# Optimization experiments

Measured on AMD Instinct MI355X. Metric: run time of the kernel, lower is better.

Reference implementation:

```python
import jax, jax.numpy as jnp
import numpy as np

NUM_HEADS = 8
SPLIT = 2  # split_size; idx=0 -> H_sp=H, W_sp=SPLIT (horizontal stripes)


def setup_inputs() -> dict:
    key = jax.random.key(0)
    k1, k2, k3 = jax.random.split(key, 3)
    B, C, H, W = 4, 64, 128, 128
    temp = jax.random.normal(k1, (B, 3, C, H, W), dtype=jnp.float32)
    conv_w = jax.random.normal(k2, (C, 1, 3, 3), dtype=jnp.float32) * 0.1  # depthwise OIHW
    conv_b = jax.random.normal(k3, (C,), dtype=jnp.float32) * 0.1
    return {"temp": temp, "conv_w": conv_w, "conv_b": conv_b}


def reference(temp, conv_w, conv_b):
    B, _, C, H, W = temp.shape
    hd = C // NUM_HEADS
    scale = hd ** (-0.5)
    H_sp, W_sp = H, SPLIT  # idx == 0

    # symmetric pad to multiples of window size (faithful to original; zero here)
    H_pad = (H_sp - H % H_sp) % H_sp
    W_pad = (W_sp - W % W_sp) % W_sp
    top, left = H_pad // 2, W_pad // 2
    x = jnp.pad(temp, ((0, 0), (0, 0), (0, 0), (top, H_pad - top), (left, W_pad - left)))
    H_, W_ = H + H_pad, W + W_pad
    q, k, v = x[:, 0], x[:, 1], x[:, 2]  # each [B,C,H_,W_]

    nW = (H_ // H_sp) * (W_ // W_sp)
    N = H_sp * W_sp  # tokens per window

    def im2cswin(t):
        # [B,C,H_,W_] -> [B*nW, heads, N, hd]
        w = t.reshape(B, C, H_ // H_sp, H_sp, W_ // W_sp, W_sp)
        w = w.transpose(0, 2, 4, 3, 5, 1).reshape(-1, N, C)
        return w.reshape(-1, N, NUM_HEADS, hd).transpose(0, 2, 1, 3)

    qh = im2cswin(q) * scale
    kh = im2cswin(k)

    # v windows as images [B*nW, C, H_sp, W_sp] for depthwise LePE conv
    vw = v.reshape(B, C, H_ // H_sp, H_sp, W_ // W_sp, W_sp)
    vw = vw.transpose(0, 2, 4, 1, 3, 5).reshape(-1, C, H_sp, W_sp)
    rpe = jax.lax.conv_general_dilated(
        vw, conv_w, window_strides=(1, 1), padding='SAME',
        feature_group_count=C, dimension_numbers=('NCHW', 'OIHW', 'NCHW'))
    rpe = rpe + conv_b[None, :, None, None]

    vh = vw.reshape(-1, NUM_HEADS, hd, N).transpose(0, 1, 3, 2)    # [B*nW,h,N,hd]
    rpeh = rpe.reshape(-1, NUM_HEADS, hd, N).transpose(0, 1, 3, 2)

    attn = jax.nn.softmax(jnp.einsum('whnd,whmd->whnm', qh, kh), axis=-1)
    out = jnp.einsum('whnm,whmd->whnd', attn, vh) + rpeh           # [B*nW,h,N,hd]

    out = out.transpose(0, 2, 1, 3).reshape(-1, N, C)              # [B*nW,N,C]
    # windows2img + crop
    out = out.reshape(B, H_ // H_sp, W_ // W_sp, H_sp, W_sp, C)
    out = out.transpose(0, 1, 3, 2, 4, 5).reshape(B, H_, W_, C)
    out = out[:, top:H + top, left:W + left, :]
    return out.reshape(B, H * W, C)
```

## Files before the change

### kernel.cpp

```cpp
#include <hip/hip_runtime.h>
#include <hip/hip_bf16.h>
#include <stdint.h>


typedef __attribute__((ext_vector_type(8))) short bf16x8;
typedef __attribute__((ext_vector_type(4))) short bf16x4;
typedef __attribute__((ext_vector_type(4))) float f32x4;

static __device__ __forceinline__ uint32_t pk2(float x, float y) {
    union { __hip_bfloat162 h2; uint32_t u; } c;
    c.h2 = __float22bfloat162_rn(make_float2(x, y));
    return c.u;
}
static __device__ __forceinline__ float bflo(uint32_t u){ return __uint_as_float(u<<16); }
static __device__ __forceinline__ float bfhi(uint32_t u){ return __uint_as_float(u & 0xffff0000u); }

static __device__ __forceinline__ f32x4 mfma16x16x16bf16(bf16x4 a, bf16x4 b, f32x4 c) {
#if __has_builtin(__builtin_amdgcn_mfma_f32_16x16x16bf16_1k)
    return __builtin_amdgcn_mfma_f32_16x16x16bf16_1k(a, b, c, 0, 0, 0);
#else
    f32x4 d;
    asm volatile("v_mfma_f32_16x16x16_bf16 %0, %1, %2, %3\n\ts_nop 7\n\ts_nop 7"
                 : "=v"(d) : "v"(a), "v"(b), "v"(c));
    return d;
#endif
}

__global__ __launch_bounds__(256, 2)
void lepe_attn(const float* __restrict__ temp,
               const float* __restrict__ conv_w,
               const float* __restrict__ conv_b,
               float* __restrict__ out)
{
    __shared__ __align__(16) char smem[55328];
    char* q_s = smem;
    char* k_s = smem + 18432;
    char* v_t = smem + 36864;
    float* cw_s = (float*)(smem + 54016);

    const int tid  = threadIdx.x;
    const int wave = tid >> 6, lane = tid & 63;
    const int lr = lane & 15, quad = lane >> 4;

    const int bid = blockIdx.x;
    const int x  = bid & 7;
    int t_ = bid >> 3;
    const int hf = t_ & 1;  t_ >>= 1;
    const int wj = t_ & 7;
    const int b  = t_ >> 3;
    const int wi = x * 8 + wj;
    const int c0 = hf * 32;

    const size_t cstr = 16384, sstr = 64 * cstr;
    const float qs = 0.35355339059327373f * 1.4426950408889634f;

    {
        const int cg = tid & 31, hh0 = tid >> 5;
        const float* qp = temp + (size_t)b*3*sstr + (size_t)(c0+cg)*cstr + wi*2;
        #pragma unroll
        for (int i = 0; i < 16; ++i) {
            int h = i*8 + hh0;
            float2 fq = *(const float2*)(qp + (size_t)h*128);
            uint32_t uq = pk2(fq.x*qs, fq.y*qs);
            *(uint16_t*)(q_s + (2*h)*72   + cg*2) = (uint16_t)uq;
            *(uint16_t*)(q_s + (2*h+1)*72 + cg*2) = (uint16_t)(uq>>16);
            float2 fk = *(const float2*)(qp + sstr + (size_t)h*128);
            uint32_t uk = pk2(fk.x, fk.y);
            *(uint16_t*)(k_s + (2*h)*72   + cg*2) = (uint16_t)uk;
            *(uint16_t*)(k_s + (2*h+1)*72 + cg*2) = (uint16_t)(uk>>16);
            float2 fv = *(const float2*)(qp + 2*sstr + (size_t)h*128);
            *(uint32_t*)(v_t + cg*536 + 4*h + 4) = pk2(fv.x, fv.y);
        }
        for (int j = tid; j < 288; j += 256) cw_s[j] = conv_w[c0*9 + j];
        if (tid < 32) {
            *(uint32_t*)(v_t + tid*536)       = 0;
            *(uint32_t*)(v_t + tid*536 + 516) = 0;
            cw_s[288 + tid] = conv_b[c0 + tid];
        }
    }
    __syncthreads();

    const f32x4 zf = {0.f, 0.f, 0.f, 0.f};
    uint4 kf[16]; uint2 vf[16];
    #pragma unroll
    for (int T = 0; T < 16; ++T) {
        uint4 kk = *(const uint4*)(k_s + (T*16 + lr)*72 + wave*16);
        kf[T] = (lane < 16) ? kk : make_uint4(0,0,0,0);
        uint2 vv = *(const uint2*)(v_t + (wave*8 + (lane&7))*536 + 4 + (T*16 + quad*4)*2);
        vf[T] = (lr < 8) ? vv : make_uint2(0,0);
    }
    __syncthreads();

    {
        const int ch = tid & 31, seg = tid >> 5;
        const char* base = v_t + ch*536 + seg*64;
        uint32_t d[18];
        *(uint4*)(d+0)  = *(const uint4*)(base);
        *(uint4*)(d+4)  = *(const uint4*)(base+16);
        *(uint4*)(d+8)  = *(const uint4*)(base+32);
        *(uint4*)(d+12) = *(const uint4*)(base+48);
        *(uint2*)(d+16) = *(const uint2*)(base+64);
        float w9[9];
        #pragma unroll
        for (int k = 0; k < 9; ++k) w9[k] = cw_s[ch*9 + k];
        const float bia = cw_s[288 + ch];
        #pragma unroll
        for (int tt = 0; tt < 32; ++tt) {
            int tok = seg*32 + tt;
            int w01 = tok & 1;
            int L = (tt >> 1) * 2;
            float rp = bia;
            #pragma unroll
            for (int dy = 0; dy < 3; ++dy) {
                #pragma unroll
                for (int wp = 0; wp < 2; ++wp) {
                    int idx = L + 2*dy + wp;
                    uint32_t dw = d[idx >> 1];
                    float tap = (idx & 1) ? bfhi(dw) : bflo(dw);
                    rp = fmaf(w9[dy*3 + wp + 1 - w01], tap, rp);
                }
            }
            union { __hip_bfloat16 h; uint16_t u; } cv;
            cv.h = __float2bfloat16(rp);
            *(uint16_t*)(k_s + tok*72 + ch*2) = cv.u;
        }
    }
    __syncthreads();

    #pragma unroll 1
    for (int qg = 0; qg < 16; ++qg) {
        uint4 qq = *(const uint4*)(q_s + (qg*16 + lr)*72 + wave*16);
        union { uint4 u; bf16x8 h8; } qf; qf.u = (lane < 16) ? qq : make_uint4(0,0,0,0);
        f32x4 acc = zf;
        float rsum = 0.f;
        #pragma unroll
        for (int T = 0; T < 16; ++T) {
            union { uint4 u; bf16x8 h8; } kfu; kfu.u = kf[T];
            f32x4 sc = __builtin_amdgcn_mfma_f32_16x16x32_bf16(kfu.h8, qf.h8, zf, 0, 0, 0);
            float e0 = __builtin_amdgcn_exp2f(sc[0]);
            float e1 = __builtin_amdgcn_exp2f(sc[1]);
            float e2 = __builtin_amdgcn_exp2f(sc[2]);
            float e3 = __builtin_amdgcn_exp2f(sc[3]);
            rsum += (e0 + e1) + (e2 + e3);
            union { uint2 u; bf16x4 h4; } pb; pb.u = make_uint2(pk2(e0,e1), pk2(e2,e3));
            union { uint2 u; bf16x4 h4; } vfu; vfu.u = vf[T];
            acc = mfma16x16x16bf16(vfu.h4, pb.h4, acc);
        }
        float rs = rsum;
        rs += __shfl_xor(rs, 16);
        rs += __shfl_xor(rs, 32);
        const float rinv = __builtin_amdgcn_rcpf(rs);
        if (quad < 2) {
            int tok = qg*16 + lr;
            int h = tok >> 1, w01 = tok & 1;
            uint2 rp2 = *(const uint2*)(k_s + tok*72 + (wave*8 + quad*4)*2);
            float4 ov;
            ov.x = fmaf(acc[0], rinv, bflo(rp2.x));
            ov.y = fmaf(acc[1], rinv, bfhi(rp2.x));
            ov.z = fmaf(acc[2], rinv, bflo(rp2.y));
            ov.w = fmaf(acc[3], rinv, bfhi(rp2.y));
            size_t addr = (size_t)b*1048576 + (size_t)(h*128 + wi*2 + w01)*64
                        + c0 + wave*8 + quad*4;
            *(float4*)(out + addr) = ov;
        }
    }
}

extern "C" void kernel_launch(void* const* d_in, const int* in_sizes, int n_in,
                              void* d_out, int out_size, void* d_ws, size_t ws_size,
                              hipStream_t stream) {
    const float* temp = (const float*)d_in[0];
    const float* cw   = (const float*)d_in[1];
    const float* cb   = (const float*)d_in[2];
    float* o = (float*)d_out;
    (void)in_sizes; (void)n_in; (void)out_size; (void)d_ws; (void)ws_size;
    lepe_attn<<<dim3(512), dim3(256), 0, stream>>>(temp, cw, cb, o);
}
```

Measured before the change: 131.8 us.

## Double block to 512 threads, split queries across wave pairs, use K=32 PV MFMA

The block grows to 8 waves, so each head is handled by two waves that each own half the query groups. Q fragments are kept in registers while K and V are streamed from shared memory, and the P·V product moves from 16x16x16 to 16x16x32 MFMA by pairing two key tiles. The LePE conv result goes to its own shared buffer, which removes one barrier and the reuse of k_s. Per-thread global load work is halved and more waves are available to hide latency. The cost is more shared memory, 8 accumulators per thread, and a 4-blocks-per-CU launch bound that may limit registers.

```diff
diff --git a/kernel.cpp b/kernel.cpp
--- a/kernel.cpp
+++ b/kernel.cpp
@@ -4,7 +4,6 @@
 
 
 typedef __attribute__((ext_vector_type(8))) short bf16x8;
-typedef __attribute__((ext_vector_type(4))) short bf16x4;
 typedef __attribute__((ext_vector_type(4))) float f32x4;
 
 static __device__ __forceinline__ uint32_t pk2(float x, float y) {
@@ -15,32 +14,23 @@
 static __device__ __forceinline__ float bflo(uint32_t u){ return __uint_as_float(u<<16); }
 static __device__ __forceinline__ float bfhi(uint32_t u){ return __uint_as_float(u & 0xffff0000u); }
 
-static __device__ __forceinline__ f32x4 mfma16x16x16bf16(bf16x4 a, bf16x4 b, f32x4 c) {
-#if __has_builtin(__builtin_amdgcn_mfma_f32_16x16x16bf16_1k)
-    return __builtin_amdgcn_mfma_f32_16x16x16bf16_1k(a, b, c, 0, 0, 0);
-#else
-    f32x4 d;
-    asm volatile("v_mfma_f32_16x16x16_bf16 %0, %1, %2, %3\n\ts_nop 7\n\ts_nop 7"
-                 : "=v"(d) : "v"(a), "v"(b), "v"(c));
-    return d;
-#endif
-}
-
-__global__ __launch_bounds__(256, 2)
+__global__ __launch_bounds__(512, 4)
 void lepe_attn(const float* __restrict__ temp,
                const float* __restrict__ conv_w,
                const float* __restrict__ conv_b,
                float* __restrict__ out)
 {
-    __shared__ __align__(16) char smem[55328];
+    __shared__ __align__(16) char smem[73728];
     char* q_s = smem;
     char* k_s = smem + 18432;
-    char* v_t = smem + 36864;
-    float* cw_s = (float*)(smem + 54016);
+    char* r_s = smem + 36864;
+    char* v_t = smem + 55296;
+    float* cw_s = (float*)(smem + 72448);
 
     const int tid  = threadIdx.x;
     const int wave = tid >> 6, lane = tid & 63;
     const int lr = lane & 15, quad = lane >> 4;
+    const int head = wave >> 1, qbase = (wave & 1) * 8;
 
     const int bid = blockIdx.x;
     const int x  = bid & 7;
@@ -58,8 +48,8 @@
         const int cg = tid & 31, hh0 = tid >> 5;
         const float* qp = temp + (size_t)b*3*sstr + (size_t)(c0+cg)*cstr + wi*2;
         #pragma unroll
-        for (int i = 0; i < 16; ++i) {
-            int h = i*8 + hh0;
+        for (int i = 0; i < 8; ++i) {
+            int h = i*16 + hh0;
             float2 fq = *(const float2*)(qp + (size_t)h*128);
             uint32_t uq = pk2(fq.x*qs, fq.y*qs);
             *(uint16_t*)(q_s + (2*h)*72   + cg*2) = (uint16_t)uq;
@@ -69,46 +59,40 @@
             *(uint16_t*)(k_s + (2*h)*72   + cg*2) = (uint16_t)uk;
             *(uint16_t*)(k_s + (2*h+1)*72 + cg*2) = (uint16_t)(uk>>16);
             float2 fv = *(const float2*)(qp + 2*sstr + (size_t)h*128);
-            *(uint32_t*)(v_t + cg*536 + 4*h + 4) = pk2(fv.x, fv.y);
+            *(uint32_t*)(v_t + cg*536 + 8 + 4*h) = pk2(fv.x, fv.y);
         }
-        for (int j = tid; j < 288; j += 256) cw_s[j] = conv_w[c0*9 + j];
+        if (tid < 288) cw_s[tid] = conv_w[c0*9 + tid];
         if (tid < 32) {
-            *(uint32_t*)(v_t + tid*536)       = 0;
-            *(uint32_t*)(v_t + tid*536 + 516) = 0;
             cw_s[288 + tid] = conv_b[c0 + tid];
+            *(uint32_t*)(v_t + tid*536 + 4)   = 0;
+            *(uint32_t*)(v_t + tid*536 + 520) = 0;
         }
     }
     __syncthreads();
 
-    const f32x4 zf = {0.f, 0.f, 0.f, 0.f};
-    uint4 kf[16]; uint2 vf[16];
+    const uint4 z4 = make_uint4(0,0,0,0);
+    uint4 qf[8];
     #pragma unroll
-    for (int T = 0; T < 16; ++T) {
-        uint4 kk = *(const uint4*)(k_s + (T*16 + lr)*72 + wave*16);
-        kf[T] = (lane < 16) ? kk : make_uint4(0,0,0,0);
-        uint2 vv = *(const uint2*)(v_t + (wave*8 + (lane&7))*536 + 4 + (T*16 + quad*4)*2);
-        vf[T] = (lr < 8) ? vv : make_uint2(0,0);
+    for (int g = 0; g < 8; ++g) {
+        uint4 t = *(const uint4*)(q_s + ((qbase+g)*16 + lr)*72 + head*16);
+        qf[g] = (lane < 16) ? t : z4;
     }
-    __syncthreads();
 
     {
         const int ch = tid & 31, seg = tid >> 5;
-        const char* base = v_t + ch*536 + seg*64;
-        uint32_t d[18];
-        *(uint4*)(d+0)  = *(const uint4*)(base);
-        *(uint4*)(d+4)  = *(const uint4*)(base+16);
-        *(uint4*)(d+8)  = *(const uint4*)(base+32);
-        *(uint4*)(d+12) = *(const uint4*)(base+48);
-        *(uint2*)(d+16) = *(const uint2*)(base+64);
+        const char* base = v_t + ch*536 + seg*32;
+        uint32_t d[12];
+        #pragma unroll
+        for (int i = 0; i < 6; ++i) *(uint2*)(d + 2*i) = *(const uint2*)(base + 8*i);
         float w9[9];
         #pragma unroll
         for (int k = 0; k < 9; ++k) w9[k] = cw_s[ch*9 + k];
         const float bia = cw_s[288 + ch];
         #pragma unroll
-        for (int tt = 0; tt < 32; ++tt) {
-            int tok = seg*32 + tt;
-            int w01 = tok & 1;
-            int L = (tt >> 1) * 2;
+        for (int tt = 0; tt < 16; ++tt) {
+            int tok = seg*16 + tt;
+            int w01 = tt & 1;
+            int L = (tt >> 1)*2 + 2;
             float rp = bia;
             #pragma unroll
             for (int dy = 0; dy < 3; ++dy) {
@@ -116,51 +100,73 @@
                 for (int wp = 0; wp < 2; ++wp) {
                     int idx = L + 2*dy + wp;
                     uint32_t dw = d[idx >> 1];
-                    float tap = (idx & 1) ? bfhi(dw) : bflo(dw);
-                    rp = fmaf(w9[dy*3 + wp + 1 - w01], tap, rp);
+                    rp = fmaf(w9[dy*3 + wp + 1 - w01], (idx&1) ? bfhi(dw) : bflo(dw), rp);
                 }
             }
             union { __hip_bfloat16 h; uint16_t u; } cv;
             cv.h = __float2bfloat16(rp);
-            *(uint16_t*)(k_s + tok*72 + ch*2) = cv.u;
+            *(uint16_t*)(r_s + tok*72 + ch*2) = cv.u;
         }
     }
     __syncthreads();
 
-    #pragma unroll 1
-    for (int qg = 0; qg < 16; ++qg) {
-        uint4 qq = *(const uint4*)(q_s + (qg*16 + lr)*72 + wave*16);
-        union { uint4 u; bf16x8 h8; } qf; qf.u = (lane < 16) ? qq : make_uint4(0,0,0,0);
-        f32x4 acc = zf;
-        float rsum = 0.f;
+    const f32x4 zf = {0.f, 0.f, 0.f, 0.f};
+    f32x4 acc[8];
+    float rsum[8];
+    #pragma unroll
+    for (int g = 0; g < 8; ++g) { acc[g] = zf; rsum[g] = 0.f; }
+
+    const char* kbase = k_s + lr*72 + head*16;
+    const char* vbase = v_t + (head*8 + (lane&7))*536 + 8 + quad*8;
+
+    #pragma unroll 2
+    for (int T = 0; T < 8; ++T) {
+        uint4 ka = *(const uint4*)(kbase + (T*32)*72);
+        uint4 kb = *(const uint4*)(kbase + (T*32+16)*72);
+        union { uint4 u; bf16x8 h; } kfa, kfb;
+        kfa.u = (lane < 16) ? ka : z4;
+        kfb.u = (lane < 16) ? kb : z4;
+        uint2 vlo = *(const uint2*)(vbase + T*64);
+        uint2 vhi = *(const uint2*)(vbase + T*64 + 32);
+        union { uint4 u; bf16x8 h; } vf;
+        vf.u = (lr < 8) ? make_uint4(vlo.x, vlo.y, vhi.x, vhi.y) : z4;
         #pragma unroll
-        for (int T = 0; T < 16; ++T) {
-            union { uint4 u; bf16x8 h8; } kfu; kfu.u = kf[T];
-            f32x4 sc = __builtin_amdgcn_mfma_f32_16x16x32_bf16(kfu.h8, qf.h8, zf, 0, 0, 0);
-            float e0 = __builtin_amdgcn_exp2f(sc[0]);
-            float e1 = __builtin_amdgcn_exp2f(sc[1]);
-            float e2 = __builtin_amdgcn_exp2f(sc[2]);
-            float e3 = __builtin_amdgcn_exp2f(sc[3]);
-            rsum += (e0 + e1) + (e2 + e3);
-            union { uint2 u; bf16x4 h4; } pb; pb.u = make_uint2(pk2(e0,e1), pk2(e2,e3));
-            union { uint2 u; bf16x4 h4; } vfu; vfu.u = vf[T];
-            acc = mfma16x16x16bf16(vfu.h4, pb.h4, acc);
+        for (int g = 0; g < 8; ++g) {
+            union { uint4 u; bf16x8 h; } qa; qa.u = qf[g];
+            f32x4 sa = __builtin_amdgcn_mfma_f32_16x16x32_bf16(kfa.h, qa.h, zf, 0, 0, 0);
+            f32x4 sb = __builtin_amdgcn_mfma_f32_16x16x32_bf16(kfb.h, qa.h, zf, 0, 0, 0);
+            float e0 = __builtin_amdgcn_exp2f(sa[0]);
+            float e1 = __builtin_amdgcn_exp2f(sa[1]);
+            float e2 = __builtin_amdgcn_exp2f(sa[2]);
+            float e3 = __builtin_amdgcn_exp2f(sa[3]);
+            float f0 = __builtin_amdgcn_exp2f(sb[0]);
+            float f1 = __builtin_amdgcn_exp2f(sb[1]);
+            float f2 = __builtin_amdgcn_exp2f(sb[2]);
+            float f3 = __builtin_amdgcn_exp2f(sb[3]);
+            rsum[g] += ((e0+e1)+(e2+e3)) + ((f0+f1)+(f2+f3));
+            union { uint4 u; bf16x8 h; } pb;
+            pb.u = make_uint4(pk2(e0,e1), pk2(e2,e3), pk2(f0,f1), pk2(f2,f3));
+            acc[g] = __builtin_amdgcn_mfma_f32_16x16x32_bf16(vf.h, pb.h, acc[g], 0, 0, 0);
         }
-        float rs = rsum;
+    }
+
+    #pragma unroll
+    for (int g = 0; g < 8; ++g) {
+        float rs = rsum[g];
         rs += __shfl_xor(rs, 16);
         rs += __shfl_xor(rs, 32);
-        const float rinv = __builtin_amdgcn_rcpf(rs);
+        const float rinv = 1.0f / rs;
         if (quad < 2) {
-            int tok = qg*16 + lr;
+            int tok = (qbase + g)*16 + lr;
             int h = tok >> 1, w01 = tok & 1;
-            uint2 rp2 = *(const uint2*)(k_s + tok*72 + (wave*8 + quad*4)*2);
+            uint2 rp2 = *(const uint2*)(r_s + tok*72 + (head*8 + quad*4)*2);
             float4 ov;
-            ov.x = fmaf(acc[0], rinv, bflo(rp2.x));
-            ov.y = fmaf(acc[1], rinv, bfhi(rp2.x));
-            ov.z = fmaf(acc[2], rinv, bflo(rp2.y));
-            ov.w = fmaf(acc[3], rinv, bfhi(rp2.y));
+            ov.x = fmaf(acc[g][0], rinv, bflo(rp2.x));
+            ov.y = fmaf(acc[g][1], rinv, bfhi(rp2.x));
+            ov.z = fmaf(acc[g][2], rinv, bflo(rp2.y));
+            ov.w = fmaf(acc[g][3], rinv, bfhi(rp2.y));
             size_t addr = (size_t)b*1048576 + (size_t)(h*128 + wi*2 + w01)*64
-                        + c0 + wave*8 + quad*4;
+                        + c0 + head*8 + quad*4;
             *(float4*)(out + addr) = ov;
         }
     }
@@ -174,5 +180,5 @@
     const float* cb   = (const float*)d_in[2];
     float* o = (float*)d_out;
     (void)in_sizes; (void)n_in; (void)out_size; (void)d_ws; (void)ws_size;
-    lepe_attn<<<dim3(512), dim3(256), 0, stream>>>(temp, cw, cb, o);
+    lepe_attn<<<dim3(512), dim3(512), 0, stream>>>(temp, cw, cb, o);
 }
```

Result: slower. 158.5 us (+20.3%).
